# Kernel optimization log

Measured on AMD Instinct MI355X. Metric: run time of the kernel, lower is better.

Reference implementation:

```python
import jax, jax.numpy as jnp
import numpy as np

B, T, H, E = 64, 48, 512, 512   # batch, max_length, hidden_size, embed_size (must equal H)
ATT, AF, FC, V = 196, 2048, 2048, 10000  # att_size, att_feat_size, fc_feat_size, vocab


def setup_inputs() -> dict:
    key = jax.random.key(0)
    ks = jax.random.split(key, 26)
    stdv = 1.0 / np.sqrt(H)

    def u(k, shape):
        return jax.random.uniform(k, shape, jnp.float32, -stdv, stdv)

    return {
        "word_idx": jax.random.randint(ks[0], (B, T), 0, V),
        "father_idx": jax.random.randint(ks[1], (B, T), 0, T),
        "fc_feats": jax.random.normal(ks[2], (B, FC), jnp.float32),
        "att_feats": jax.random.normal(ks[3], (B, ATT, AF), jnp.float32),
        # fc_embed / att_embed / word embedding
        "W_fc": u(ks[4], (E, FC)), "b_fc": u(ks[5], (E,)),
        "W_att": u(ks[6], (E, AF)), "b_att": u(ks[7], (E,)),
        "embed_tab": u(ks[8], (V, E)),
        # MDLSTMCell parameters
        "weight_f1": u(ks[9], (H, E + H)), "bias_f1": u(ks[10], (H,)),
        "weight_f2": u(ks[11], (H, E + H)), "bias_f2": u(ks[12], (H,)),
        "weight_H": u(ks[13], (2 * H, 2 * E + 2 * H)), "bias_H": u(ks[14], (2 * H,)),
        "weight_I": u(ks[15], (H, 2 * E + 2 * H + AF)), "bias_I": u(ks[16], (H,)),
        # attention core
        "W_ha": u(ks[17], (H, H)), "b_ha": u(ks[18], (H,)),
        "W_hf": u(ks[19], (H, H)), "b_hf": u(ks[20], (H,)),
        "W_alpha": u(ks[21], (1, H)), "b_alpha": u(ks[22], (1,)),
        # output logit
        "W_logit": u(ks[23], (V, H)), "b_logit": u(ks[24], (V,)),
    }


def _forward(word_idx, father_idx, fc_feats, att_feats,
             W_fc, b_fc, W_att, b_att, embed_tab,
             weight_f1, bias_f1, weight_f2, bias_f2,
             weight_H, bias_H, weight_I, bias_I,
             W_ha, b_ha, W_hf, b_hf, W_alpha, b_alpha,
             W_logit, b_logit):
    Bn, Tn = word_idx.shape
    Hd = weight_f1.shape[0]

    fc_emb = fc_feats @ W_fc.T + b_fc                 # [B, E]
    p_att = att_feats @ W_att.T + b_att               # [B, ATT, H]
    att_mean = att_feats.mean(axis=1)                 # [B, AF]
    barange = jnp.arange(Bn)

    def attention(ha, hf):
        # dot: [B, ATT, H]
        dot = jnp.tanh((ha @ W_ha.T + b_ha)[:, None, :]
                       + (hf @ W_hf.T + b_hf)[:, None, :] + p_att)
        logits = (dot @ W_alpha.T + b_alpha)[..., 0]  # [B, ATT]
        w = jax.nn.softmax(logits, axis=1)
        return jnp.einsum('ba,bad->bd', w, att_feats)  # [B, AF]

    def cell(x1, x2, h1, c1, h2, c2, att_res):
        cat = jnp.concatenate([x1, x2, h1, h2], axis=1)
        gates = cat @ weight_H.T + bias_H
        ingate, outgate = jnp.split(gates, 2, axis=1)
        ingate = jax.nn.sigmoid(ingate)
        outgate = jax.nn.sigmoid(outgate)
        cat_hat = jnp.concatenate([x1, x2, h1, h2, att_res], axis=1)
        cellgate = jnp.tanh(cat_hat @ weight_I.T + bias_I)
        f1 = jax.nn.sigmoid(jnp.concatenate([x1, h1], axis=1) @ weight_f1.T + bias_f1)
        f2 = jax.nn.sigmoid(jnp.concatenate([x2, h2], axis=1) @ weight_f2.T + bias_f2)
        nc = f1 * c1 + f2 * c2 + ingate * cellgate
        nh = outgate * jnp.tanh(nc)
        return nh, nc

    def step(carry, i):
        h_states, c_states = carry                    # each [B, T, H]
        father = father_idx[:, i]
        is_first = (i == 0)
        # ancestor branch (gathered from father position)
        w_a = word_idx[barange, father]
        x_a = jnp.where(is_first, fc_emb, embed_tab[w_a])
        h_a = jnp.where(is_first, 0.0, h_states[barange, father])
        c_a = jnp.where(is_first, 0.0, c_states[barange, father])
        # sibling branch (previous timestep, reset when (i-1) % 3 == 0)
        ip = jnp.maximum(i - 1, 0)
        use_f = jnp.logical_not(is_first | (((i - 1) % 3) == 0))
        x_f = jnp.where(use_f, embed_tab[word_idx[:, ip]], 0.0)
        h_f = jnp.where(use_f, h_states[:, ip], 0.0)
        c_f = jnp.where(use_f, c_states[:, ip], 0.0)
        att_res = jnp.where(is_first, att_mean, attention(h_a, h_f))
        nh, nc = cell(x_a, x_f, h_a, c_a, h_f, c_f, att_res)
        h_states = jax.lax.dynamic_update_slice(h_states, nh[:, None, :], (0, i, 0))
        c_states = jax.lax.dynamic_update_slice(c_states, nc[:, None, :], (0, i, 0))
        return (h_states, c_states), nh

    init = (jnp.zeros((Bn, Tn, Hd), jnp.float32), jnp.zeros((Bn, Tn, Hd), jnp.float32))
    _, outs = jax.lax.scan(step, init, jnp.arange(Tn))
    outs = jnp.transpose(outs, (1, 0, 2))             # [B, T, H]
    logits = outs @ W_logit.T + b_logit               # [B, T, V]
    return jax.nn.log_softmax(logits, axis=2)


def reference(word_idx, father_idx, fc_feats, att_feats,
              W_fc, b_fc, W_att, b_att, embed_tab,
              weight_f1, bias_f1, weight_f2, bias_f2,
              weight_H, bias_H, weight_I, bias_I,
              W_ha, b_ha, W_hf, b_hf, W_alpha, b_alpha,
              W_logit, b_logit):
    return _forward(word_idx, father_idx, fc_feats, att_feats,
                    W_fc, b_fc, W_att, b_att, embed_tab,
                    weight_f1, bias_f1, weight_f2, bias_f2,
                    weight_H, bias_H, weight_I, bias_I,
                    W_ha, b_ha, W_hf, b_hf, W_alpha, b_alpha,
                    W_logit, b_logit)
```

## Files before the change

kernel.cpp:

```cpp
#include <hip/hip_runtime.h>
#include <hip/hip_bf16.h>
#include <type_traits>

#define B_   64
#define T_   48
#define H_   512
#define E_   512
#define ATT_ 196
#define AF_  2048
#define FC_  2048
#define V_   10000

typedef unsigned short u16;
typedef unsigned int u32;
using s16x8 = __attribute__((ext_vector_type(8))) short;
using f32x4 = __attribute__((ext_vector_type(4))) float;

#define MD_BF16 0
#define MD_F32  1
#define MD_DYN  2

__device__ __forceinline__ float b2f(u16 u) {
  union { unsigned int i; float f; } x; x.i = ((unsigned int)u) << 16; return x.f;
}
__device__ __forceinline__ u16 f2b(float f) {
  union { float f; unsigned int i; } x; x.f = f;
  unsigned int r = x.i + 0x7fffu + ((x.i >> 16) & 1u);
  return (u16)(r >> 16);
}
__device__ __forceinline__ float sigmoid_(float x) { return 1.f / (1.f + __expf(-x)); }
__device__ __forceinline__ float tanh_(float x) { return 1.f - 2.f / (__expf(2.f * x) + 1.f); }

__device__ __forceinline__ float ldf(const void* p, size_t i, int f) {
  return f ? ((const float*)p)[i] : b2f(((const u16*)p)[i]);
}
__device__ __forceinline__ s16x8 ld8(const void* p, size_t idx, int f) {
  s16x8 r;
  if (f) {
    const float* q = (const float*)p + idx;
    float4 x = *(const float4*)q;
    float4 y = *(const float4*)(q + 4);
    r[0] = (short)f2b(x.x); r[1] = (short)f2b(x.y);
    r[2] = (short)f2b(x.z); r[3] = (short)f2b(x.w);
    r[4] = (short)f2b(y.x); r[5] = (short)f2b(y.y);
    r[6] = (short)f2b(y.z); r[7] = (short)f2b(y.w);
  } else {
    r = *(const s16x8*)((const u16*)p + idx);
  }
  return r;
}
__device__ __forceinline__ s16x8 zero8() {
  s16x8 r; for (int j = 0; j < 8; j++) r[j] = 0; return r;
}

__global__ void detect_f32(const u16* __restrict__ p, int* __restrict__ flag) {
  __shared__ int sb[256];
  int t = threadIdx.x, bad = 0;
  for (int i = t; i < 65536; i += 256) {
    int e = (p[i] >> 7) & 0xFF;
    bad |= (e == 0xFF) ? 1 : 0;
  }
  sb[t] = bad; __syncthreads();
  for (int s = 128; s; s >>= 1) { if (t < s) sb[t] |= sb[t + s]; __syncthreads(); }
  if (t == 0) *flag = sb[0];
}

template <typename CT>
__global__ __launch_bounds__(256) void gemm_nt(
    const void* __restrict__ A, int lda, size_t aoff, int amode,
    const void* __restrict__ B, int ldb, size_t boff, int bmode,
    CT* __restrict__ C, int ldc, int N, int Kc,
    const float* __restrict__ bias, size_t zstride, const int* __restrict__ flagp)
{
  __shared__ __align__(16) u16 As[64 * 40];
  __shared__ __align__(16) u16 Bs[64 * 40];

  const int dynf = *flagp;
  const int aF = (amode == MD_DYN) ? dynf : amode;
  const int bF = (bmode == MD_DYN) ? dynf : bmode;

  const int tid  = threadIdx.x;
  const int m0   = blockIdx.x * 64;
  const int n0   = blockIdx.y * 64;
  const int kz   = blockIdx.z * Kc;
  const int lane = tid & 63;
  const int w    = tid >> 6;
  const int wm   = (w >> 1) * 32;
  const int wn   = (w & 1) * 32;
  const int quad = lane >> 4;
  const int r16  = lane & 15;

  f32x4 acc[2][2];
  for (int a = 0; a < 2; a++) for (int b = 0; b < 2; b++)
    for (int k = 0; k < 4; k++) acc[a][b][k] = 0.f;

  const int sr = tid >> 2;
  const int sc = (tid & 3) * 8;
  const size_t idxA = (size_t)(m0 + sr) * lda + aoff + kz + sc;
  const size_t idxB = (size_t)(n0 + sr) * ldb + boff + kz + sc;
  const bool bok = (n0 + sr) < N;

  const int aoff0 = (wm + r16) * 40 + quad * 8;
  const int aoff1 = (wm + 16 + r16) * 40 + quad * 8;
  const int boff0 = (wn + r16) * 40 + quad * 8;
  const int boff1 = (wn + 16 + r16) * 40 + quad * 8;

  s16x8 av = ld8(A, idxA, aF);
  s16x8 bv = bok ? ld8(B, idxB, bF) : zero8();

  for (int k0 = 0; k0 < Kc; k0 += 32) {
    s16x8 avn = zero8(), bvn = zero8();
    if (k0 + 32 < Kc) {
      avn = ld8(A, idxA + k0 + 32, aF);
      if (bok) bvn = ld8(B, idxB + k0 + 32, bF);
    }
    __syncthreads();
    *(s16x8*)(As + sr * 40 + sc) = av;
    *(s16x8*)(Bs + sr * 40 + sc) = bv;
    __syncthreads();
    s16x8 a0 = *(const s16x8*)(As + aoff0);
    s16x8 a1 = *(const s16x8*)(As + aoff1);
    s16x8 b0 = *(const s16x8*)(Bs + boff0);
    s16x8 b1 = *(const s16x8*)(Bs + boff1);
    acc[0][0] = __builtin_amdgcn_mfma_f32_16x16x32_bf16(a0, b0, acc[0][0], 0, 0, 0);
    acc[0][1] = __builtin_amdgcn_mfma_f32_16x16x32_bf16(a0, b1, acc[0][1], 0, 0, 0);
    acc[1][0] = __builtin_amdgcn_mfma_f32_16x16x32_bf16(a1, b0, acc[1][0], 0, 0, 0);
    acc[1][1] = __builtin_amdgcn_mfma_f32_16x16x32_bf16(a1, b1, acc[1][1], 0, 0, 0);
    av = avn; bv = bvn;
  }

  CT* Cz = C + (size_t)blockIdx.z * zstride;
  const bool addb = (bias != nullptr) && (blockIdx.z == 0);
  for (int tm = 0; tm < 2; tm++)
    for (int tn = 0; tn < 2; tn++) {
      int col = n0 + wn + tn * 16 + r16;
      if (col >= N) continue;
      float bb = addb ? bias[col] : 0.f;
      int rowbase = m0 + wm + tm * 16 + quad * 4;
      for (int rg = 0; rg < 4; rg++) {
        float v = acc[tm][tn][rg] + bb;
        if constexpr (std::is_same<CT, float>::value)
          Cz[(size_t)(rowbase + rg) * ldc + col] = v;
        else
          Cz[(size_t)(rowbase + rg) * ldc + col] = f2b(v);
      }
    }
}

__global__ __launch_bounds__(256) void step_pre(
    const u16* __restrict__ hcat,
    const u16* __restrict__ WstepH, const float* __restrict__ biasStep,
    float* __restrict__ Gbuf,
    const u16* __restrict__ Whahf, const float* __restrict__ bhahf,
    float* __restrict__ tatf, int do_tat)
{
  __shared__ __align__(16) u16 As[64 * 40];
  __shared__ __align__(16) u16 Bs[64 * 40];

  const int tid = threadIdx.x;
  const int blk = blockIdx.x;
  const int lane = tid & 63;
  const int w    = tid >> 6;
  const int wm   = (w >> 1) * 32;
  const int wn   = (w & 1) * 32;
  const int quad = lane >> 4;
  const int r16  = lane & 15;

  const u16* Bb; float* Cc; const float* bias;
  int kz, Kc, ldc, n0; bool addb;
  if (blk < 80) {
    const int by = blk % 40, bz = blk / 40;
    n0 = by * 64; kz = bz * 512; Kc = 512; ldc = 2560;
    Bb = WstepH; Cc = Gbuf + (size_t)bz * (B_ * 2560);
    bias = biasStep; addb = (bz == 0);
  } else {
    if (!do_tat) return;
    n0 = (blk - 80) * 64; kz = 0; Kc = 1024; ldc = 512;
    Bb = Whahf; Cc = tatf; bias = bhahf; addb = true;
  }

  f32x4 acc[2][2];
  for (int a = 0; a < 2; a++) for (int c = 0; c < 2; c++)
    for (int k = 0; k < 4; k++) acc[a][c][k] = 0.f;

  const int sr = tid >> 2;
  const int sc = (tid & 3) * 8;
  const u16* pa = hcat + (size_t)sr * 1024 + kz + sc;
  const u16* pb = Bb + (size_t)(n0 + sr) * 1024 + kz + sc;

  const int ao0 = (wm + r16) * 40 + quad * 8;
  const int ao1 = (wm + 16 + r16) * 40 + quad * 8;
  const int bo0 = (wn + r16) * 40 + quad * 8;
  const int bo1 = (wn + 16 + r16) * 40 + quad * 8;

  s16x8 av = *(const s16x8*)pa;
  s16x8 bv = *(const s16x8*)pb;

  for (int k0 = 0; k0 < Kc; k0 += 32) {
    s16x8 avn = zero8(), bvn = zero8();
    if (k0 + 32 < Kc) {
      avn = *(const s16x8*)(pa + k0 + 32);
      bvn = *(const s16x8*)(pb + k0 + 32);
    }
    __syncthreads();
    *(s16x8*)(As + sr * 40 + sc) = av;
    *(s16x8*)(Bs + sr * 40 + sc) = bv;
    __syncthreads();
    s16x8 a0 = *(const s16x8*)(As + ao0);
    s16x8 a1 = *(const s16x8*)(As + ao1);
    s16x8 b0 = *(const s16x8*)(Bs + bo0);
    s16x8 b1 = *(const s16x8*)(Bs + bo1);
    acc[0][0] = __builtin_amdgcn_mfma_f32_16x16x32_bf16(a0, b0, acc[0][0], 0, 0, 0);
    acc[0][1] = __builtin_amdgcn_mfma_f32_16x16x32_bf16(a0, b1, acc[0][1], 0, 0, 0);
    acc[1][0] = __builtin_amdgcn_mfma_f32_16x16x32_bf16(a1, b0, acc[1][0], 0, 0, 0);
    acc[1][1] = __builtin_amdgcn_mfma_f32_16x16x32_bf16(a1, b1, acc[1][1], 0, 0, 0);
    av = avn; bv = bvn;
  }

  for (int tm = 0; tm < 2; tm++)
    for (int tn = 0; tn < 2; tn++) {
      int col = n0 + wn + tn * 16 + r16;
      float bb = addb ? bias[col] : 0.f;
      int rowbase = wm + tm * 16 + quad * 4;
      for (int rg = 0; rg < 4; rg++)
        Cc[(size_t)(rowbase + rg) * ldc + col] = acc[tm][tn][rg] + bb;
    }
}

__global__ __launch_bounds__(512) void att_fin(
    const float* __restrict__ tatf, const u16* __restrict__ p_att,
    const float* __restrict__ walpha_f, const u16* __restrict__ att_proj,
    const float* __restrict__ att_meanp,
    const float* __restrict__ Gbuf, const float* __restrict__ Gx,
    float* __restrict__ c_states, u16* __restrict__ houts,
    u16* __restrict__ hcat, const int* __restrict__ father_idx, int i)
{
  __shared__ float tat_sh[512];
  __shared__ float sl[256];
  __shared__ float red[512];

  const int b = blockIdx.x, tid = threadIdx.x;
  const int lane = tid & 63, w = tid >> 6;
  const int is_first = (i == 0);
  const int use_f = (!is_first) && ((i - 1) % 3 != 0);

  float attv;
  if (is_first) {
    attv = att_meanp[b * H_ + tid];
  } else {
    tat_sh[tid] = tatf[b * H_ + tid];
    __syncthreads();
    {
      float t8[8], wa8[8];
#pragma unroll
      for (int j = 0; j < 8; j++) {
        t8[j]  = tat_sh[lane * 8 + j];
        wa8[j] = walpha_f[lane * 8 + j];
      }
      const u16* pb = p_att + (size_t)b * ATT_ * 512 + lane * 8;
      s16x8 pv = *(const s16x8*)(pb + (size_t)w * 512);
      for (int a = w; a < ATT_; a += 8) {
        s16x8 nx = zero8();
        if (a + 8 < ATT_) nx = *(const s16x8*)(pb + (size_t)(a + 8) * 512);
        float acc = 0.f;
#pragma unroll
        for (int j = 0; j < 8; j++)
          acc += wa8[j] * tanh_(t8[j] + b2f((u16)pv[j]));
#pragma unroll
        for (int off = 32; off; off >>= 1) acc += __shfl_down(acc, off);
        if (lane == 0) sl[a] = acc;
        pv = nx;
      }
    }
    __syncthreads();
    float l = (tid < ATT_) ? sl[tid] : -3.0e38f;
    red[tid] = l; __syncthreads();
    for (int s = 256; s; s >>= 1) { if (tid < s) red[tid] = fmaxf(red[tid], red[tid + s]); __syncthreads(); }
    float mx = red[0]; __syncthreads();
    float e = (tid < ATT_) ? __expf(l - mx) : 0.f;
    red[tid] = e; __syncthreads();
    for (int s = 256; s; s >>= 1) { if (tid < s) red[tid] += red[tid + s]; __syncthreads(); }
    float inv = 1.f / red[0];
    __syncthreads();
    if (tid < ATT_) sl[tid] = e * inv;
    __syncthreads();
    {
      const u16* ap = att_proj + (size_t)b * ATT_ * 512 + tid;
      float ac0 = 0.f, ac1 = 0.f, ac2 = 0.f, ac3 = 0.f;
      for (int a = 0; a < ATT_; a += 4) {
        ac0 += sl[a]     * b2f(ap[(size_t)a * 512]);
        ac1 += sl[a + 1] * b2f(ap[(size_t)(a + 1) * 512]);
        ac2 += sl[a + 2] * b2f(ap[(size_t)(a + 2) * 512]);
        ac3 += sl[a + 3] * b2f(ap[(size_t)(a + 3) * 512]);
      }
      attv = (ac0 + ac1) + (ac2 + ac3);
    }
  }

  const size_t zs = (size_t)B_ * 2560;
  const float* Gb = Gbuf + (size_t)b * 2560 + tid;
  const float* gx = Gx + ((size_t)i * B_ + b) * 2560 + tid;
  float g0 = Gb[0]    + Gb[zs];
  float g1 = Gb[512]  + Gb[zs + 512];
  float g2 = Gb[1024] + Gb[zs + 1024];
  float g3 = Gb[1536] + Gb[zs + 1536];
  float g4 = Gb[2048] + Gb[zs + 2048];
  float ing  = sigmoid_(g0 + gx[0]);
  float outg = sigmoid_(g1 + gx[512]);
  float cg   = tanh_(g2 + gx[1024] + attv);
  float f1   = sigmoid_(g3 + gx[1536]);
  float f2   = sigmoid_(g4 + gx[2048]);
  const int father = father_idx[b * T_ + i];
  float c1 = is_first ? 0.f : c_states[((size_t)b * T_ + father) * H_ + tid];
  float c2 = use_f ? c_states[((size_t)b * T_ + (i - 1)) * H_ + tid] : 0.f;
  float nc = f1 * c1 + f2 * c2 + ing * cg;
  float nh = outg * tanh_(nc);
  size_t o = ((size_t)b * T_ + i) * H_ + tid;
  c_states[o] = nc;
  u16 hb = f2b(nh);
  houts[o] = hb;
  if (i + 1 < T_) {
    const int fn = father_idx[b * T_ + (i + 1)];
    const int use_fn = (i % 3 != 0);
    u16 ha = (fn == i) ? hb : houts[((size_t)b * T_ + fn) * H_ + tid];
    hcat[(size_t)b * 1024 + tid] = ha;
    hcat[(size_t)b * 1024 + 512 + tid] = use_fn ? hb : (u16)0;
  }
}

__global__ __launch_bounds__(256) void pack_wstep(
    const void* __restrict__ wH, const void* __restrict__ wI,
    const void* __restrict__ wf1, const void* __restrict__ wf2,
    u16* __restrict__ WstepX, u16* __restrict__ WstepH,
    const int* __restrict__ flagp)
{
  const int F = *flagp;
  for (int idx = blockIdx.x * 256 + threadIdx.x; idx < 2560 * 2048; idx += gridDim.x * 256) {
    int row = idx >> 11, col = idx & 2047;
    float v = 0.f;
    if (row < 1024) v = ldf(wH, (size_t)row * 2048 + col, F);
    else if (row < 1536) v = ldf(wI, (size_t)(row - 1024) * 4096 + col, F);
    else if (row < 2048) {
      int r = row - 1536;
      if (col < 512) v = ldf(wf1, (size_t)r * 1024 + col, F);
      else if (col >= 1024 && col < 1536) v = ldf(wf1, (size_t)r * 1024 + 512 + (col - 1024), F);
    } else {
      int r = row - 2048;
      if (col >= 512 && col < 1024) v = ldf(wf2, (size_t)r * 1024 + (col - 512), F);
      else if (col >= 1536) v = ldf(wf2, (size_t)r * 1024 + 512 + (col - 1536), F);
    }
    if (col < 1024) WstepX[(size_t)row * 1024 + col] = f2b(v);
    else           WstepH[(size_t)row * 1024 + (col - 1024)] = f2b(v);
  }
}

__global__ __launch_bounds__(256) void pack_whahf(
    const void* __restrict__ W_ha, const void* __restrict__ W_hf,
    u16* __restrict__ Whahf, const int* __restrict__ flagp)
{
  const int F = *flagp;
  for (int idx = blockIdx.x * 256 + threadIdx.x; idx < 512 * 1024; idx += gridDim.x * 256) {
    int e = idx >> 10, k = idx & 1023;
    float v = (k < 512) ? ldf(W_ha, (size_t)e * 512 + k, F)
                        : ldf(W_hf, (size_t)e * 512 + (k - 512), F);
    Whahf[idx] = f2b(v);
  }
}

__global__ __launch_bounds__(256) void pack_attf(
    const void* __restrict__ src, u16* __restrict__ dst, const int* __restrict__ flagp)
{
  const int F = *flagp;
  const size_t n8 = (size_t)B_ * ATT_ * AF_ / 8;
  for (size_t idx = (size_t)blockIdx.x * 256 + threadIdx.x; idx < n8;
       idx += (size_t)gridDim.x * 256) {
    s16x8 v = ld8(src, idx * 8, F);
    *(s16x8*)(dst + idx * 8) = v;
  }
}

__global__ __launch_bounds__(256) void pack_xall(
    const float* __restrict__ fc_emb, const void* __restrict__ embed_tab,
    const int* __restrict__ word_idx, const int* __restrict__ father_idx,
    u16* __restrict__ XAll, const int* __restrict__ flagp)
{
  const int F = *flagp;
  const int ib = blockIdx.x;
  const int i = ib >> 6, b = ib & 63;
  u16* xr = XAll + (size_t)ib * 1024;
  const int fa = father_idx[b * T_ + i];
  const int wa = word_idx[b * T_ + fa];
  const int use_f = (i > 0 && ((i - 1) % 3 != 0));
  const int wf = (i > 0) ? word_idx[b * T_ + (i - 1)] : 0;
  for (int rep = 0; rep < 2; ++rep) {
    int c = threadIdx.x + rep * 256;
    xr[c] = (i == 0) ? f2b(fc_emb[b * E_ + c])
                     : f2b(ldf(embed_tab, (size_t)wa * E_ + c, F));
    xr[512 + c] = use_f ? f2b(ldf(embed_tab, (size_t)wf * E_ + c, F)) : (u16)0;
  }
}

__global__ __launch_bounds__(256) void pack_bias(
    const void* bH, const void* bI, const void* bf1, const void* bf2,
    const void* bha, const void* bhf, const void* batt, const void* bfc,
    const void* blogit, const void* Walpha,
    float* biasStep, float* bhahf, float* batt_f, float* bfc_f, float* blogit_f,
    float* walpha_f, const int* __restrict__ flagp)
{
  const int F = *flagp;
  int t = blockIdx.x * 256 + threadIdx.x;
  if (t < 1024) biasStep[t] = ldf(bH, t, F);
  else if (t < 1536) biasStep[t] = ldf(bI, t - 1024, F);
  else if (t < 2048) biasStep[t] = ldf(bf1, t - 1536, F);
  else if (t < 2560) biasStep[t] = ldf(bf2, t - 2048, F);
  if (t < 512) {
    bhahf[t] = ldf(bha, t, F) + ldf(bhf, t, F);
    batt_f[t] = ldf(batt, t, F);
    bfc_f[t] = ldf(bfc, t, F);
    walpha_f[t] = ldf(Walpha, t, F);
  }
  if (t < V_) blogit_f[t] = ldf(blogit, t, F);
}

__global__ __launch_bounds__(256) void att_apply_kernel(
    const float* __restrict__ alog, const u16* __restrict__ att_proj,
    float* __restrict__ outc)
{
  int b = blockIdx.x, seg = blockIdx.y, tid = threadIdx.x;
  __shared__ float sw[ATT_];
  __shared__ float rb[256];
  if (alog) {
    float l = (tid < ATT_) ? alog[b * ATT_ + tid] : -3.0e38f;
    rb[tid] = l; __syncthreads();
    for (int s = 128; s; s >>= 1) { if (tid < s) rb[tid] = fmaxf(rb[tid], rb[tid + s]); __syncthreads(); }
    float mx = rb[0]; __syncthreads();
    float e = (tid < ATT_) ? __expf(l - mx) : 0.f;
    rb[tid] = e; __syncthreads();
    for (int s = 128; s; s >>= 1) { if (tid < s) rb[tid] += rb[tid + s]; __syncthreads(); }
    float sum = rb[0]; __syncthreads();
    if (tid < ATT_) sw[tid] = e / sum;
  } else {
    if (tid < ATT_) sw[tid] = 1.f / (float)ATT_;
  }
  __syncthreads();
  int lane = tid & 63, g = tid >> 6;
  int col = seg * 64 + lane;
  float acc = 0.f;
  for (int a = g; a < ATT_; a += 4)
    acc += sw[a] * b2f(att_proj[(size_t)(b * ATT_ + a) * H_ + col]);
  rb[tid] = acc; __syncthreads();
  if (g == 0) outc[b * H_ + col] = rb[lane] + rb[64 + lane] + rb[128 + lane] + rb[192 + lane];
}

__global__ __launch_bounds__(256) void logsoftmax_kernel(float* __restrict__ out)
{
  __shared__ float vals[V_];
  __shared__ float rb[256];
  int row = blockIdx.x, tid = threadIdx.x;
  float* p = out + (size_t)row * V_;
  float mx = -3.0e38f;
  for (int c = tid * 4; c < V_; c += 1024) {
    float4 q = *(const float4*)(p + c);
    vals[c] = q.x; vals[c + 1] = q.y; vals[c + 2] = q.z; vals[c + 3] = q.w;
    mx = fmaxf(mx, fmaxf(fmaxf(q.x, q.y), fmaxf(q.z, q.w)));
  }
  rb[tid] = mx; __syncthreads();
  for (int s = 128; s; s >>= 1) { if (tid < s) rb[tid] = fmaxf(rb[tid], rb[tid + s]); __syncthreads(); }
  mx = rb[0]; __syncthreads();
  float sum = 0.f;
  for (int c = tid; c < V_; c += 256) sum += __expf(vals[c] - mx);
  rb[tid] = sum; __syncthreads();
  for (int s = 128; s; s >>= 1) { if (tid < s) rb[tid] += rb[tid + s]; __syncthreads(); }
  float lse = mx + __logf(rb[0]);
  for (int c = tid * 4; c < V_; c += 1024) {
    float4 q;
    q.x = vals[c] - lse; q.y = vals[c + 1] - lse;
    q.z = vals[c + 2] - lse; q.w = vals[c + 3] - lse;
    *(float4*)(p + c) = q;
  }
}

extern "C" void kernel_launch(void* const* d_in, const int* in_sizes, int n_in,
                              void* d_out, int out_size, void* d_ws, size_t ws_size,
                              hipStream_t stream)
{
  const int* word_idx   = (const int*)d_in[0];
  const int* father_idx = (const int*)d_in[1];
  const void* fc_feats  = d_in[2];
  const void* att_feats = d_in[3];
  const void* W_fc      = d_in[4];
  const void* b_fc      = d_in[5];
  const void* W_att     = d_in[6];
  const void* b_att     = d_in[7];
  const void* embed_tab = d_in[8];
  const void* weight_f1 = d_in[9];
  const void* bias_f1   = d_in[10];
  const void* weight_f2 = d_in[11];
  const void* bias_f2   = d_in[12];
  const void* weight_H  = d_in[13];
  const void* bias_H    = d_in[14];
  const void* weight_I  = d_in[15];
  const void* bias_I    = d_in[16];
  const void* W_ha      = d_in[17];
  const void* b_ha      = d_in[18];
  const void* W_hf      = d_in[19];
  const void* b_hf      = d_in[20];
  const void* W_alpha   = d_in[21];
  const void* b_alpha   = d_in[22];
  const void* W_logit   = d_in[23];
  const void* b_logit   = d_in[24];
  (void)b_alpha;

  char* dob = (char*)d_out;
  size_t doff = 0;
  auto oalloc = [&](size_t bytes) -> char* {
    char* p = dob + doff;
    doff += (bytes + 255) & ~(size_t)255;
    return p;
  };
  u16*  p_att    = (u16*)oalloc((size_t)B_ * ATT_ * E_ * 2);
  u16*  att_proj = (u16*)oalloc((size_t)B_ * ATT_ * H_ * 2);
  u16*  att_bf16 = (u16*)oalloc((size_t)B_ * ATT_ * AF_ * 2);
  float* Gx       = (float*)att_bf16;
  u16*  WstepX   = (u16*)oalloc((size_t)2560 * 1024 * 2);
  u16*  WstepH   = (u16*)oalloc((size_t)2560 * 1024 * 2);
  u16*  Whahf    = (u16*)oalloc((size_t)512 * 1024 * 2);
  u16*  XAll     = (u16*)oalloc((size_t)B_ * T_ * 1024 * 2);
  float* c_states = (float*)oalloc((size_t)B_ * T_ * H_ * 4);
  float* Gbuf     = (float*)oalloc((size_t)2 * B_ * 2560 * 4);
  u16*  hcat     = (u16*)oalloc((size_t)B_ * 1024 * 2);
  float* tatf     = (float*)oalloc((size_t)B_ * H_ * 4);
  float* fc_emb   = (float*)oalloc((size_t)B_ * E_ * 4);
  float* att_meanp= (float*)oalloc((size_t)B_ * H_ * 4);
  float* biasStep = (float*)oalloc(2560 * 4);
  float* bhahf    = (float*)oalloc(512 * 4);
  float* batt_f   = (float*)oalloc(512 * 4);
  float* bfc_f    = (float*)oalloc(512 * 4);
  float* walpha_f = (float*)oalloc(512 * 4);

  char* ws = (char*)d_ws;
  size_t woff = 0;
  auto walloc = [&](size_t bytes) -> char* {
    char* p = ws + woff;
    woff += (bytes + 255) & ~(size_t)255;
    return p;
  };
  u16*  houts     = (u16*)walloc((size_t)B_ * T_ * H_ * 2);
  float* blogit_f = (float*)walloc((size_t)V_ * 4);
  int*   flag     = (int*)walloc(256);

  hipMemsetAsync(c_states, 0, (size_t)B_ * T_ * H_ * 4, stream);
  hipMemsetAsync(houts, 0, (size_t)B_ * T_ * H_ * 2, stream);
  hipMemsetAsync(hcat, 0, (size_t)B_ * 1024 * 2, stream);

  detect_f32<<<1, 256, 0, stream>>>((const u16*)att_feats, flag);

  pack_wstep<<<4096, 256, 0, stream>>>(weight_H, weight_I, weight_f1, weight_f2,
                                       WstepX, WstepH, flag);
  pack_whahf<<<2048, 256, 0, stream>>>(W_ha, W_hf, Whahf, flag);
  pack_attf<<<4096, 256, 0, stream>>>(att_feats, att_bf16, flag);
  pack_bias<<<40, 256, 0, stream>>>(bias_H, bias_I, bias_f1, bias_f2, b_ha, b_hf,
                                    b_att, b_fc, b_logit, W_alpha,
                                    biasStep, bhahf, batt_f, bfc_f, blogit_f,
                                    walpha_f, flag);

  gemm_nt<float><<<dim3(1, 8, 1), 256, 0, stream>>>(
      fc_feats, FC_, 0, MD_DYN, W_fc, FC_, 0, MD_DYN,
      fc_emb, E_, E_, FC_, bfc_f, 0, flag);
  pack_xall<<<B_ * T_, 256, 0, stream>>>(fc_emb, embed_tab, word_idx, father_idx,
                                         XAll, flag);
  gemm_nt<u16><<<dim3(B_ * ATT_ / 64, 8, 1), 256, 0, stream>>>(
      att_bf16, AF_, 0, MD_BF16, W_att, AF_, 0, MD_DYN,
      p_att, E_, E_, AF_, batt_f, 0, flag);
  gemm_nt<u16><<<dim3(B_ * ATT_ / 64, 8, 1), 256, 0, stream>>>(
      att_bf16, AF_, 0, MD_BF16, weight_I, 4096, 2048, MD_DYN,
      att_proj, H_, H_, AF_, nullptr, 0, flag);
  gemm_nt<float><<<dim3(B_ * T_ / 64, 2560 / 64, 1), 256, 0, stream>>>(
      XAll, 1024, 0, MD_BF16, WstepX, 1024, 0, MD_BF16,
      Gx, 2560, 2560, 1024, nullptr, 0, flag);
  att_apply_kernel<<<dim3(B_, 8), 256, 0, stream>>>(nullptr, att_proj, att_meanp);

  for (int i = 0; i < T_; ++i) {
    step_pre<<<88, 256, 0, stream>>>(hcat, WstepH, biasStep, Gbuf,
                                     Whahf, bhahf, tatf, i > 0 ? 1 : 0);
    att_fin<<<B_, 512, 0, stream>>>(tatf, p_att, walpha_f, att_proj, att_meanp,
                                    Gbuf, Gx, c_states, houts, hcat,
                                    father_idx, i);
  }

  gemm_nt<float><<<dim3(B_ * T_ / 64, (V_ + 63) / 64, 1), 256, 0, stream>>>(
      houts, H_, 0, MD_BF16, W_logit, H_, 0, MD_DYN,
      (float*)d_out, V_, V_, H_, blogit_f, 0, flag);
  logsoftmax_kernel<<<B_ * T_, 256, 0, stream>>>((float*)d_out);
}
```

Before: 3.195 ms.

## Fuse recurrent step into one kernel with intra-launch atomic barrier

Each recurrent step now uses a single launch, where before it took two (step_pre plus att_fin). 64 blocks do the attention and cell update and write hcat. The other 48 blocks prefetch combined weights, spin on an atomic counter until the cell blocks finish, then compute the next step's gate and attention pre-activations into a ping-pong buffer. This halves the per-step launches and overlaps weight prefetch with the cell work. The cost is a spin-wait that relies on all 112 blocks being co-resident. The logit GEMM also moves to a dedicated kernel with XCD-aware block swizzling.

```diff
diff --git a/kernel.cpp b/kernel.cpp
--- a/kernel.cpp
+++ b/kernel.cpp
@@ -10,9 +10,11 @@
 #define AF_  2048
 #define FC_  2048
 #define V_   10000
+#define GB_N 3072
 
 typedef unsigned short u16;
 typedef unsigned int u32;
+typedef unsigned long long u64;
 using s16x8 = __attribute__((ext_vector_type(8))) short;
 using f32x4 = __attribute__((ext_vector_type(4))) float;
 
@@ -51,6 +53,19 @@
 }
 __device__ __forceinline__ s16x8 zero8() {
   s16x8 r; for (int j = 0; j < 8; j++) r[j] = 0; return r;
+}
+
+__device__ __forceinline__ u64 aload_u64(const u64* p) {
+  return __hip_atomic_load(p, __ATOMIC_RELAXED, __HIP_MEMORY_SCOPE_AGENT);
+}
+__device__ __forceinline__ void astore_u32(u32* p, u32 v) {
+  __hip_atomic_store(p, v, __ATOMIC_RELAXED, __HIP_MEMORY_SCOPE_AGENT);
+}
+__device__ __forceinline__ s16x8 ld8_coh(const u16* p) {
+  union { u64 u[2]; s16x8 v; } x;
+  x.u[0] = aload_u64((const u64*)p);
+  x.u[1] = aload_u64((const u64*)p + 1);
+  return x.v;
 }
 
 __global__ void detect_f32(const u16* __restrict__ p, int* __restrict__ flag) {
@@ -147,18 +162,22 @@
     }
 }
 
-__global__ __launch_bounds__(256) void step_pre(
-    const u16* __restrict__ hcat,
-    const u16* __restrict__ WstepH, const float* __restrict__ biasStep,
-    float* __restrict__ Gbuf,
-    const u16* __restrict__ Whahf, const float* __restrict__ bhahf,
-    float* __restrict__ tatf, int do_tat)
+__global__ __launch_bounds__(256) void gemm_logit(
+    const u16* __restrict__ A, const void* __restrict__ B,
+    float* __restrict__ C, const float* __restrict__ bias,
+    const int* __restrict__ flagp)
 {
   __shared__ __align__(16) u16 As[64 * 40];
   __shared__ __align__(16) u16 Bs[64 * 40];
 
-  const int tid = threadIdx.x;
-  const int blk = blockIdx.x;
+  const int bF = *flagp;
+  const int bid = blockIdx.x;
+  const int xcd = bid & 7, rest = bid >> 3;
+  const int yl = rest % 20, xt = rest / 20;
+  const int m0 = xt * 64;
+  const int n0 = (xcd * 20 + yl) * 64;
+
+  const int tid  = threadIdx.x;
   const int lane = tid & 63;
   const int w    = tid >> 6;
   const int wm   = (w >> 1) * 32;
@@ -166,27 +185,15 @@
   const int quad = lane >> 4;
   const int r16  = lane & 15;
 
-  const u16* Bb; float* Cc; const float* bias;
-  int kz, Kc, ldc, n0; bool addb;
-  if (blk < 80) {
-    const int by = blk % 40, bz = blk / 40;
-    n0 = by * 64; kz = bz * 512; Kc = 512; ldc = 2560;
-    Bb = WstepH; Cc = Gbuf + (size_t)bz * (B_ * 2560);
-    bias = biasStep; addb = (bz == 0);
-  } else {
-    if (!do_tat) return;
-    n0 = (blk - 80) * 64; kz = 0; Kc = 1024; ldc = 512;
-    Bb = Whahf; Cc = tatf; bias = bhahf; addb = true;
-  }
-
   f32x4 acc[2][2];
-  for (int a = 0; a < 2; a++) for (int c = 0; c < 2; c++)
-    for (int k = 0; k < 4; k++) acc[a][c][k] = 0.f;
+  for (int a = 0; a < 2; a++) for (int b = 0; b < 2; b++)
+    for (int k = 0; k < 4; k++) acc[a][b][k] = 0.f;
 
   const int sr = tid >> 2;
   const int sc = (tid & 3) * 8;
-  const u16* pa = hcat + (size_t)sr * 1024 + kz + sc;
-  const u16* pb = Bb + (size_t)(n0 + sr) * 1024 + kz + sc;
+  const u16* pa = A + (size_t)(m0 + sr) * 512 + sc;
+  const size_t idxB = (size_t)(n0 + sr) * 512 + sc;
+  const bool bok = (n0 + sr) < V_;
 
   const int ao0 = (wm + r16) * 40 + quad * 8;
   const int ao1 = (wm + 16 + r16) * 40 + quad * 8;
@@ -194,13 +201,13 @@
   const int bo1 = (wn + 16 + r16) * 40 + quad * 8;
 
   s16x8 av = *(const s16x8*)pa;
-  s16x8 bv = *(const s16x8*)pb;
-
-  for (int k0 = 0; k0 < Kc; k0 += 32) {
+  s16x8 bv = bok ? ld8(B, idxB, bF) : zero8();
+
+  for (int k0 = 0; k0 < 512; k0 += 32) {
     s16x8 avn = zero8(), bvn = zero8();
-    if (k0 + 32 < Kc) {
+    if (k0 + 32 < 512) {
       avn = *(const s16x8*)(pa + k0 + 32);
-      bvn = *(const s16x8*)(pb + k0 + 32);
+      if (bok) bvn = ld8(B, idxB + k0 + 32, bF);
     }
     __syncthreads();
     *(s16x8*)(As + sr * 40 + sc) = av;
@@ -220,118 +227,235 @@
   for (int tm = 0; tm < 2; tm++)
     for (int tn = 0; tn < 2; tn++) {
       int col = n0 + wn + tn * 16 + r16;
-      float bb = addb ? bias[col] : 0.f;
-      int rowbase = wm + tm * 16 + quad * 4;
+      if (col >= V_) continue;
+      float bb = bias[col];
+      int rowbase = m0 + wm + tm * 16 + quad * 4;
       for (int rg = 0; rg < 4; rg++)
-        Cc[(size_t)(rowbase + rg) * ldc + col] = acc[tm][tn][rg] + bb;
-    }
-}
-
-__global__ __launch_bounds__(512) void att_fin(
-    const float* __restrict__ tatf, const u16* __restrict__ p_att,
-    const float* __restrict__ walpha_f, const u16* __restrict__ att_proj,
-    const float* __restrict__ att_meanp,
-    const float* __restrict__ Gbuf, const float* __restrict__ Gx,
+        C[(size_t)(rowbase + rg) * V_ + col] = acc[tm][tn][rg] + bb;
+    }
+}
+
+__global__ __launch_bounds__(512) void ginit(float* __restrict__ G,
+                                             const float* __restrict__ biasComb)
+{
+  const size_t idx = (size_t)blockIdx.x * 512 + threadIdx.x;
+  const int c = (int)(idx % GB_N);
+  G[idx] = biasComb[c];
+  G[(size_t)B_ * GB_N + idx] = 0.f;
+}
+
+__global__ __launch_bounds__(512) void step_full(
+    const float* __restrict__ Gprev, float* __restrict__ Gnext,
+    const u16* __restrict__ p_att, const float* __restrict__ walpha_f,
+    const u16* __restrict__ att_proj, const float* __restrict__ att_meanp,
+    const float* __restrict__ Gx,
     float* __restrict__ c_states, u16* __restrict__ houts,
-    u16* __restrict__ hcat, const int* __restrict__ father_idx, int i)
-{
-  __shared__ float tat_sh[512];
-  __shared__ float sl[256];
-  __shared__ float red[512];
-
-  const int b = blockIdx.x, tid = threadIdx.x;
+    u16* __restrict__ hcat, const int* __restrict__ father_idx,
+    const u16* __restrict__ Wcomb, const float* __restrict__ biasComb,
+    int* __restrict__ barcnt, int btarget, int i)
+{
+  const int blk = blockIdx.x, tid = threadIdx.x;
   const int lane = tid & 63, w = tid >> 6;
-  const int is_first = (i == 0);
-  const int use_f = (!is_first) && ((i - 1) % 3 != 0);
-
-  float attv;
-  if (is_first) {
-    attv = att_meanp[b * H_ + tid];
-  } else {
-    tat_sh[tid] = tatf[b * H_ + tid];
+  const size_t zs = (size_t)B_ * GB_N;
+
+  if (blk < 64) {
+    __shared__ float tat_sh[512];
+    __shared__ float sl[256];
+    __shared__ float red[512];
+    __shared__ u16 nh_sh[512];
+    __shared__ u16 ha_sh[512];
+
+    const int b = blk;
+    const int is_first = (i == 0);
+    const int use_f = (!is_first) && ((i - 1) % 3 != 0);
+
+    const float* Gb = Gprev + (size_t)b * GB_N + tid;
+    float g0 = Gb[0]    + Gb[zs];
+    float g1 = Gb[512]  + Gb[zs + 512];
+    float g2 = Gb[1024] + Gb[zs + 1024];
+    float g3 = Gb[1536] + Gb[zs + 1536];
+    float g4 = Gb[2048] + Gb[zs + 2048];
+    const float* gx = Gx + ((size_t)i * B_ + b) * 2560 + tid;
+    float gx0 = gx[0], gx1 = gx[512], gx2 = gx[1024];
+    float gx3 = gx[1536], gx4 = gx[2048];
+
+    float attv;
+    if (is_first) {
+      attv = att_meanp[b * H_ + tid];
+    } else {
+      tat_sh[tid] = Gb[2560] + Gb[zs + 2560];
+      __syncthreads();
+      {
+        float t8[8], wa8[8];
+#pragma unroll
+        for (int j = 0; j < 8; j++) {
+          t8[j]  = tat_sh[lane * 8 + j];
+          wa8[j] = walpha_f[lane * 8 + j];
+        }
+        const u16* pb = p_att + (size_t)b * ATT_ * 512 + lane * 8;
+        s16x8 pv = *(const s16x8*)(pb + (size_t)w * 512);
+        for (int a = w; a < ATT_; a += 8) {
+          s16x8 nx = zero8();
+          if (a + 8 < ATT_) nx = *(const s16x8*)(pb + (size_t)(a + 8) * 512);
+          float acc = 0.f;
+#pragma unroll
+          for (int j = 0; j < 8; j++)
+            acc += wa8[j] * tanh_(t8[j] + b2f((u16)pv[j]));
+#pragma unroll
+          for (int off = 32; off; off >>= 1) acc += __shfl_down(acc, off);
+          if (lane == 0) sl[a] = acc;
+          pv = nx;
+        }
+      }
+      __syncthreads();
+      float l = (tid < ATT_) ? sl[tid] : -3.0e38f;
+      red[tid] = l; __syncthreads();
+      for (int s = 256; s; s >>= 1) { if (tid < s) red[tid] = fmaxf(red[tid], red[tid + s]); __syncthreads(); }
+      float mx = red[0]; __syncthreads();
+      float e = (tid < ATT_) ? __expf(l - mx) : 0.f;
+      red[tid] = e; __syncthreads();
+      for (int s = 256; s; s >>= 1) { if (tid < s) red[tid] += red[tid + s]; __syncthreads(); }
+      float inv = 1.f / red[0];
+      __syncthreads();
+      if (tid < ATT_) sl[tid] = e * inv;
+      __syncthreads();
+      {
+        const u16* ap = att_proj + (size_t)b * ATT_ * 512 + tid;
+        float ac0 = 0.f, ac1 = 0.f, ac2 = 0.f, ac3 = 0.f;
+        for (int a = 0; a < ATT_; a += 4) {
+          ac0 += sl[a]     * b2f(ap[(size_t)a * 512]);
+          ac1 += sl[a + 1] * b2f(ap[(size_t)(a + 1) * 512]);
+          ac2 += sl[a + 2] * b2f(ap[(size_t)(a + 2) * 512]);
+          ac3 += sl[a + 3] * b2f(ap[(size_t)(a + 3) * 512]);
+        }
+        attv = (ac0 + ac1) + (ac2 + ac3);
+      }
+    }
+
+    float ing  = sigmoid_(g0 + gx0);
+    float outg = sigmoid_(g1 + gx1);
+    float cg   = tanh_(g2 + gx2 + attv);
+    float f1   = sigmoid_(g3 + gx3);
+    float f2   = sigmoid_(g4 + gx4);
+    const int father = father_idx[b * T_ + i];
+    float c1 = is_first ? 0.f : c_states[((size_t)b * T_ + father) * H_ + tid];
+    float c2 = use_f ? c_states[((size_t)b * T_ + (i - 1)) * H_ + tid] : 0.f;
+    float nc = f1 * c1 + f2 * c2 + ing * cg;
+    float nh = outg * tanh_(nc);
+    size_t o = ((size_t)b * T_ + i) * H_ + tid;
+    c_states[o] = nc;
+    u16 hb = f2b(nh);
+    houts[o] = hb;
+    if (i + 1 < T_) {
+      const int fn = father_idx[b * T_ + (i + 1)];
+      const int use_fn = (i % 3 != 0);
+      nh_sh[tid] = hb;
+      ha_sh[tid] = (fn == i) ? hb : houts[((size_t)b * T_ + fn) * H_ + tid];
+      __syncthreads();
+      if (tid < 256) {
+        u32 aw = (u32)ha_sh[2 * tid] | ((u32)ha_sh[2 * tid + 1] << 16);
+        u32 fw = use_fn ? ((u32)nh_sh[2 * tid] | ((u32)nh_sh[2 * tid + 1] << 16)) : 0u;
+        astore_u32((u32*)(hcat + (size_t)b * 1024) + tid, aw);
+        astore_u32((u32*)(hcat + (size_t)b * 1024 + 512) + tid, fw);
+      }
+    }
+    asm volatile("s_waitcnt vmcnt(0)" ::: "memory");
     __syncthreads();
-    {
-      float t8[8], wa8[8];
-#pragma unroll
-      for (int j = 0; j < 8; j++) {
-        t8[j]  = tat_sh[lane * 8 + j];
-        wa8[j] = walpha_f[lane * 8 + j];
-      }
-      const u16* pb = p_att + (size_t)b * ATT_ * 512 + lane * 8;
-      s16x8 pv = *(const s16x8*)(pb + (size_t)w * 512);
-      for (int a = w; a < ATT_; a += 8) {
-        s16x8 nx = zero8();
-        if (a + 8 < ATT_) nx = *(const s16x8*)(pb + (size_t)(a + 8) * 512);
-        float acc = 0.f;
-#pragma unroll
-        for (int j = 0; j < 8; j++)
-          acc += wa8[j] * tanh_(t8[j] + b2f((u16)pv[j]));
-#pragma unroll
-        for (int off = 32; off; off >>= 1) acc += __shfl_down(acc, off);
-        if (lane == 0) sl[a] = acc;
-        pv = nx;
-      }
-    }
+    if (tid == 0)
+      __hip_atomic_fetch_add(barcnt, 1, __ATOMIC_RELAXED, __HIP_MEMORY_SCOPE_AGENT);
+    return;
+  }
+
+  if (i + 1 >= T_) return;
+  __shared__ __align__(16) u16 As[64 * 40];
+  __shared__ __align__(16) u16 Bs[128 * 40];
+
+  const int g  = blk - 64;
+  const int ny = g % 24, z = g / 24;
+  const int n0 = ny * 128, kz = z * 512;
+  const int wm = (w & 1) * 32;
+  const int wn = (w >> 1) * 32;
+  const int quad = lane >> 4;
+  const int r16  = lane & 15;
+
+  {
+    const u16* wb = Wcomb + (size_t)n0 * 1024 + kz;
+    for (int l = tid; l < 1024; l += 512) {
+      const volatile u32* pl =
+          (const volatile u32*)(wb + (size_t)(l >> 3) * 1024 + (l & 7) * 64);
+      (void)*pl;
+    }
+  }
+  if (tid == 0) {
+    while (__hip_atomic_load(barcnt, __ATOMIC_RELAXED, __HIP_MEMORY_SCOPE_AGENT) < btarget)
+      __builtin_amdgcn_s_sleep(2);
+  }
+  __syncthreads();
+
+  const int r  = tid & 255;
+  const int sr = r >> 2;
+  const int sc = (r & 3) * 8;
+  s16x8 areg[16];
+  if (tid < 256) {
+    const u16* ap = hcat + (size_t)sr * 1024 + kz + sc;
+#pragma unroll
+    for (int it = 0; it < 16; ++it) areg[it] = ld8_coh(ap + it * 32);
+  }
+  const int br = tid >> 2;
+  const int bc = (tid & 3) * 8;
+  const u16* bp = Wcomb + (size_t)(n0 + br) * 1024 + kz + bc;
+
+  f32x4 acc[2][2];
+#pragma unroll
+  for (int a = 0; a < 2; a++)
+#pragma unroll
+    for (int c = 0; c < 2; c++)
+#pragma unroll
+      for (int k = 0; k < 4; k++) acc[a][c][k] = 0.f;
+
+  const int ao0 = (wm + r16) * 40 + quad * 8;
+  const int ao1 = (wm + 16 + r16) * 40 + quad * 8;
+  const int bo0 = (wn + r16) * 40 + quad * 8;
+  const int bo1 = (wn + 16 + r16) * 40 + quad * 8;
+
+  s16x8 bv = *(const s16x8*)bp;
+#pragma unroll
+  for (int it = 0; it < 16; ++it) {
+    s16x8 bn = zero8();
+    if (it + 1 < 16) bn = *(const s16x8*)(bp + (it + 1) * 32);
     __syncthreads();
-    float l = (tid < ATT_) ? sl[tid] : -3.0e38f;
-    red[tid] = l; __syncthreads();
-    for (int s = 256; s; s >>= 1) { if (tid < s) red[tid] = fmaxf(red[tid], red[tid + s]); __syncthreads(); }
-    float mx = red[0]; __syncthreads();
-    float e = (tid < ATT_) ? __expf(l - mx) : 0.f;
-    red[tid] = e; __syncthreads();
-    for (int s = 256; s; s >>= 1) { if (tid < s) red[tid] += red[tid + s]; __syncthreads(); }
-    float inv = 1.f / red[0];
+    if (tid < 256) *(s16x8*)(As + sr * 40 + sc) = areg[it];
+    *(s16x8*)(Bs + br * 40 + bc) = bv;
     __syncthreads();
-    if (tid < ATT_) sl[tid] = e * inv;
-    __syncthreads();
-    {
-      const u16* ap = att_proj + (size_t)b * ATT_ * 512 + tid;
-      float ac0 = 0.f, ac1 = 0.f, ac2 = 0.f, ac3 = 0.f;
-      for (int a = 0; a < ATT_; a += 4) {
-        ac0 += sl[a]     * b2f(ap[(size_t)a * 512]);
-        ac1 += sl[a + 1] * b2f(ap[(size_t)(a + 1) * 512]);
-        ac2 += sl[a + 2] * b2f(ap[(size_t)(a + 2) * 512]);
-        ac3 += sl[a + 3] * b2f(ap[(size_t)(a + 3) * 512]);
-      }
-      attv = (ac0 + ac1) + (ac2 + ac3);
-    }
-  }
-
-  const size_t zs = (size_t)B_ * 2560;
-  const float* Gb = Gbuf + (size_t)b * 2560 + tid;
-  const float* gx = Gx + ((size_t)i * B_ + b) * 2560 + tid;
-  float g0 = Gb[0]    + Gb[zs];
-  float g1 = Gb[512]  + Gb[zs + 512];
-  float g2 = Gb[1024] + Gb[zs + 1024];
-  float g3 = Gb[1536] + Gb[zs + 1536];
-  float g4 = Gb[2048] + Gb[zs + 2048];
-  float ing  = sigmoid_(g0 + gx[0]);
-  float outg = sigmoid_(g1 + gx[512]);
-  float cg   = tanh_(g2 + gx[1024] + attv);
-  float f1   = sigmoid_(g3 + gx[1536]);
-  float f2   = sigmoid_(g4 + gx[2048]);
-  const int father = father_idx[b * T_ + i];
-  float c1 = is_first ? 0.f : c_states[((size_t)b * T_ + father) * H_ + tid];
-  float c2 = use_f ? c_states[((size_t)b * T_ + (i - 1)) * H_ + tid] : 0.f;
-  float nc = f1 * c1 + f2 * c2 + ing * cg;
-  float nh = outg * tanh_(nc);
-  size_t o = ((size_t)b * T_ + i) * H_ + tid;
-  c_states[o] = nc;
-  u16 hb = f2b(nh);
-  houts[o] = hb;
-  if (i + 1 < T_) {
-    const int fn = father_idx[b * T_ + (i + 1)];
-    const int use_fn = (i % 3 != 0);
-    u16 ha = (fn == i) ? hb : houts[((size_t)b * T_ + fn) * H_ + tid];
-    hcat[(size_t)b * 1024 + tid] = ha;
-    hcat[(size_t)b * 1024 + 512 + tid] = use_fn ? hb : (u16)0;
-  }
+    s16x8 a0 = *(const s16x8*)(As + ao0);
+    s16x8 a1 = *(const s16x8*)(As + ao1);
+    s16x8 b0 = *(const s16x8*)(Bs + bo0);
+    s16x8 b1 = *(const s16x8*)(Bs + bo1);
+    acc[0][0] = __builtin_amdgcn_mfma_f32_16x16x32_bf16(a0, b0, acc[0][0], 0, 0, 0);
+    acc[0][1] = __builtin_amdgcn_mfma_f32_16x16x32_bf16(a0, b1, acc[0][1], 0, 0, 0);
+    acc[1][0] = __builtin_amdgcn_mfma_f32_16x16x32_bf16(a1, b0, acc[1][0], 0, 0, 0);
+    acc[1][1] = __builtin_amdgcn_mfma_f32_16x16x32_bf16(a1, b1, acc[1][1], 0, 0, 0);
+    bv = bn;
+  }
+
+  float* Cz = Gnext + (size_t)z * zs;
+#pragma unroll
+  for (int tm = 0; tm < 2; tm++)
+#pragma unroll
+    for (int tn = 0; tn < 2; tn++) {
+      int col = n0 + wn + tn * 16 + r16;
+      float bb = (z == 0) ? biasComb[col] : 0.f;
+      int row0 = wm + tm * 16 + quad * 4;
+#pragma unroll
+      for (int rg = 0; rg < 4; rg++)
+        Cz[(size_t)(row0 + rg) * GB_N + col] = acc[tm][tn][rg] + bb;
+    }
 }
 
 __global__ __launch_bounds__(256) void pack_wstep(
     const void* __restrict__ wH, const void* __restrict__ wI,
     const void* __restrict__ wf1, const void* __restrict__ wf2,
-    u16* __restrict__ WstepX, u16* __restrict__ WstepH,
+    u16* __restrict__ WstepX, u16* __restrict__ Wcomb,
     const int* __restrict__ flagp)
 {
   const int F = *flagp;
@@ -350,20 +474,20 @@
       else if (col >= 1536) v = ldf(wf2, (size_t)r * 1024 + 512 + (col - 1536), F);
     }
     if (col < 1024) WstepX[(size_t)row * 1024 + col] = f2b(v);
-    else           WstepH[(size_t)row * 1024 + (col - 1024)] = f2b(v);
+    else           Wcomb[(size_t)row * 1024 + (col - 1024)] = f2b(v);
   }
 }
 
 __global__ __launch_bounds__(256) void pack_whahf(
     const void* __restrict__ W_ha, const void* __restrict__ W_hf,
-    u16* __restrict__ Whahf, const int* __restrict__ flagp)
+    u16* __restrict__ Wcomb, const int* __restrict__ flagp)
 {
   const int F = *flagp;
   for (int idx = blockIdx.x * 256 + threadIdx.x; idx < 512 * 1024; idx += gridDim.x * 256) {
     int e = idx >> 10, k = idx & 1023;
     float v = (k < 512) ? ldf(W_ha, (size_t)e * 512 + k, F)
                         : ldf(W_hf, (size_t)e * 512 + (k - 512), F);
-    Whahf[idx] = f2b(v);
+    Wcomb[(size_t)2560 * 1024 + idx] = f2b(v);
   }
 }
 
@@ -404,17 +528,17 @@
     const void* bH, const void* bI, const void* bf1, const void* bf2,
     const void* bha, const void* bhf, const void* batt, const void* bfc,
     const void* blogit, const void* Walpha,
-    float* biasStep, float* bhahf, float* batt_f, float* bfc_f, float* blogit_f,
+    float* biasComb, float* batt_f, float* bfc_f, float* blogit_f,
     float* walpha_f, const int* __restrict__ flagp)
 {
   const int F = *flagp;
   int t = blockIdx.x * 256 + threadIdx.x;
-  if (t < 1024) biasStep[t] = ldf(bH, t, F);
-  else if (t < 1536) biasStep[t] = ldf(bI, t - 1024, F);
-  else if (t < 2048) biasStep[t] = ldf(bf1, t - 1536, F);
-  else if (t < 2560) biasStep[t] = ldf(bf2, t - 2048, F);
+  if (t < 1024) biasComb[t] = ldf(bH, t, F);
+  else if (t < 1536) biasComb[t] = ldf(bI, t - 1024, F);
+  else if (t < 2048) biasComb[t] = ldf(bf1, t - 1536, F);
+  else if (t < 2560) biasComb[t] = ldf(bf2, t - 2048, F);
   if (t < 512) {
-    bhahf[t] = ldf(bha, t, F) + ldf(bhf, t, F);
+    biasComb[2560 + t] = ldf(bha, t, F) + ldf(bhf, t, F);
     batt_f[t] = ldf(batt, t, F);
     bfc_f[t] = ldf(bfc, t, F);
     walpha_f[t] = ldf(Walpha, t, F);
@@ -523,17 +647,15 @@
   u16*  att_bf16 = (u16*)oalloc((size_t)B_ * ATT_ * AF_ * 2);
   float* Gx       = (float*)att_bf16;
   u16*  WstepX   = (u16*)oalloc((size_t)2560 * 1024 * 2);
-  u16*  WstepH   = (u16*)oalloc((size_t)2560 * 1024 * 2);
-  u16*  Whahf    = (u16*)oalloc((size_t)512 * 1024 * 2);
+  u16*  Wcomb    = (u16*)oalloc((size_t)GB_N * 1024 * 2);
   u16*  XAll     = (u16*)oalloc((size_t)B_ * T_ * 1024 * 2);
   float* c_states = (float*)oalloc((size_t)B_ * T_ * H_ * 4);
-  float* Gbuf     = (float*)oalloc((size_t)2 * B_ * 2560 * 4);
+  float* GbufA    = (float*)oalloc((size_t)2 * B_ * GB_N * 4);
+  float* GbufB    = (float*)oalloc((size_t)2 * B_ * GB_N * 4);
   u16*  hcat     = (u16*)oalloc((size_t)B_ * 1024 * 2);
-  float* tatf     = (float*)oalloc((size_t)B_ * H_ * 4);
   float* fc_emb   = (float*)oalloc((size_t)B_ * E_ * 4);
   float* att_meanp= (float*)oalloc((size_t)B_ * H_ * 4);
-  float* biasStep = (float*)oalloc(2560 * 4);
-  float* bhahf    = (float*)oalloc(512 * 4);
+  float* biasComb = (float*)oalloc(GB_N * 4);
   float* batt_f   = (float*)oalloc(512 * 4);
   float* bfc_f    = (float*)oalloc(512 * 4);
   float* walpha_f = (float*)oalloc(512 * 4);
@@ -548,20 +670,21 @@
   u16*  houts     = (u16*)walloc((size_t)B_ * T_ * H_ * 2);
   float* blogit_f = (float*)walloc((size_t)V_ * 4);
   int*   flag     = (int*)walloc(256);
+  int*   barws    = (int*)walloc(256);
 
   hipMemsetAsync(c_states, 0, (size_t)B_ * T_ * H_ * 4, stream);
   hipMemsetAsync(houts, 0, (size_t)B_ * T_ * H_ * 2, stream);
-  hipMemsetAsync(hcat, 0, (size_t)B_ * 1024 * 2, stream);
+  hipMemsetAsync(barws, 0, 256, stream);
 
   detect_f32<<<1, 256, 0, stream>>>((const u16*)att_feats, flag);
 
   pack_wstep<<<4096, 256, 0, stream>>>(weight_H, weight_I, weight_f1, weight_f2,
-                                       WstepX, WstepH, flag);
-  pack_whahf<<<2048, 256, 0, stream>>>(W_ha, W_hf, Whahf, flag);
+                                       WstepX, Wcomb, flag);
+  pack_whahf<<<2048, 256, 0, stream>>>(W_ha, W_hf, Wcomb, flag);
   pack_attf<<<4096, 256, 0, stream>>>(att_feats, att_bf16, flag);
   pack_bias<<<40, 256, 0, stream>>>(bias_H, bias_I, bias_f1, bias_f2, b_ha, b_hf,
                                     b_att, b_fc, b_logit, W_alpha,
-                                    biasStep, bhahf, batt_f, bfc_f, blogit_f,
+                                    biasComb, batt_f, bfc_f, blogit_f,
                                     walpha_f, flag);
 
   gemm_nt<float><<<dim3(1, 8, 1), 256, 0, stream>>>(
@@ -580,16 +703,19 @@
       Gx, 2560, 2560, 1024, nullptr, 0, flag);
   att_apply_kernel<<<dim3(B_, 8), 256, 0, stream>>>(nullptr, att_proj, att_meanp);
 
+  ginit<<<(B_ * GB_N) / 512, 512, 0, stream>>>(GbufA, biasComb);
+
+  float* Gp = GbufA;
+  float* Gn = GbufB;
   for (int i = 0; i < T_; ++i) {
-    step_pre<<<88, 256, 0, stream>>>(hcat, WstepH, biasStep, Gbuf,
-                                     Whahf, bhahf, tatf, i > 0 ? 1 : 0);
-    att_fin<<<B_, 512, 0, stream>>>(tatf, p_att, walpha_f, att_proj, att_meanp,
-                                    Gbuf, Gx, c_states, houts, hcat,
-                                    father_idx, i);
-  }
-
-  gemm_nt<float><<<dim3(B_ * T_ / 64, (V_ + 63) / 64, 1), 256, 0, stream>>>(
-      houts, H_, 0, MD_BF16, W_logit, H_, 0, MD_DYN,
-      (float*)d_out, V_, V_, H_, blogit_f, 0, flag);
+    step_full<<<112, 512, 0, stream>>>(
+        Gp, Gn, p_att, walpha_f, att_proj, att_meanp, Gx,
+        c_states, houts, hcat, father_idx, Wcomb, biasComb,
+        barws, 64 * (i + 1), i);
+    float* t = Gp; Gp = Gn; Gn = t;
+  }
+
+  gemm_logit<<<48 * 160, 256, 0, stream>>>(houts, W_logit, (float*)d_out,
+                                           blogit_f, flag);
   logsoftmax_kernel<<<B_ * T_, 256, 0, stream>>>((float*)d_out);
 }
```

After: 2.989 ms. 6.4% less time.
